# Kernel tuning notes

Measured on AMD Instinct MI355X. Metric: run time of the kernel, lower is better.

Reference implementation:

```python
import jax, jax.numpy as jnp
import numpy as np

AUX_LOSS_WEIGHT = 0.01
TOP_K = 2


def setup_inputs() -> dict:
    key = jax.random.key(0)
    k0, k1, k2, k3, k4 = jax.random.split(key, 5)
    B, S, H, I, E = 4, 2048, 1024, 2816, 8
    scale = 0.02
    x = jax.random.normal(k0, (B, S, H), dtype=jnp.float32)
    Wr = jax.random.normal(k1, (H, E), dtype=jnp.float32) * scale   # router
    Wg = jax.random.normal(k2, (E, H, I), dtype=jnp.float32) * scale  # gate proj per expert
    Wu = jax.random.normal(k3, (E, H, I), dtype=jnp.float32) * scale  # up proj per expert
    Wd = jax.random.normal(k4, (E, I, H), dtype=jnp.float32) * scale  # down proj per expert
    return {"x": x, "Wr": Wr, "Wg": Wg, "Wu": Wu, "Wd": Wd}


def reference(x, Wr, Wg, Wu, Wd):
    B, S, H = x.shape
    E = Wr.shape[1]
    xf = x.reshape(-1, H)                      # [T, H]

    # Router: softmax -> top-k -> renormalize top-k weights
    logits = xf @ Wr                           # [T, E]
    probs = jax.nn.softmax(logits, axis=-1)
    vals, idx = jax.lax.top_k(probs, TOP_K)    # [T, K]
    vals = vals / (vals.sum(axis=-1, keepdims=True) + 1e-9)

    # Aux load-balancing loss (matches torch: mean prob * mean one-hot load)
    oh = jax.nn.one_hot(idx, E, dtype=xf.dtype)        # [T, K, E]
    expert_load = oh.sum(axis=1).mean(axis=0)          # [E]
    expert_prob = probs.mean(axis=0)                   # [E]
    router_loss = E * jnp.sum(expert_prob * expert_load) * AUX_LOSS_WEIGHT

    # Per-token combine weight for each expert: c[t,e] = sum_k vals[t,k] * (idx[t,k]==e)
    comb = jnp.einsum('tk,tke->te', vals, oh)          # [T, E]

    # Loop over the small fixed set of experts (dense SwiGLU, masked-weighted combine;
    # identical math to gather -> expert -> weighted index_add scatter)
    def expert_step(acc, ew):
        wg, wu, wd, ce = ew                            # [H,I], [H,I], [I,H], [T]
        h = jax.nn.silu(xf @ wg) * (xf @ wu)           # [T, I]
        return acc + (h @ wd) * ce[:, None], None

    out, _ = jax.lax.scan(expert_step, jnp.zeros_like(xf), (Wg, Wu, Wd, comb.T))
    return out.reshape(B, S, H), router_loss
```

## Files before the change

### kernel.cpp

```cpp
#include <hip/hip_runtime.h>
#include <stdint.h>

#define T_TOK 8192
#define HD    1024
#define ID    2816
#define NE    8
#define RCAP  17408

typedef __bf16 bf16x8 __attribute__((ext_vector_type(8)));
typedef float  f32x4  __attribute__((ext_vector_type(4)));

__device__ __forceinline__ unsigned short f2bf(float f) {
  union { float f; unsigned u; } v; v.f = f;
  unsigned r = v.u + 0x7FFFu + ((v.u >> 16) & 1u);
  return (unsigned short)(r >> 16);
}

__device__ __forceinline__ void gl16(const void* g, void* l) {
  __builtin_amdgcn_global_load_lds((__attribute__((address_space(1))) void*)g,
                                   (__attribute__((address_space(3))) void*)l,
                                   16, 0, 0);
}

__global__ void k_transpose(const float* __restrict__ Wg, const float* __restrict__ Wu,
                            const float* __restrict__ Wd,
                            unsigned short* __restrict__ Wgt, unsigned short* __restrict__ Wut,
                            unsigned short* __restrict__ Wdt) {
  const int m = blockIdx.y;
  const float* src; unsigned short* dst; int R, C;
  if (m < 8)       { src = Wg + (size_t)m * HD * ID;        dst = Wgt + (size_t)m * HD * ID;        R = HD; C = ID; }
  else if (m < 16) { src = Wu + (size_t)(m - 8) * HD * ID;  dst = Wut + (size_t)(m - 8) * HD * ID;  R = HD; C = ID; }
  else             { src = Wd + (size_t)(m - 16) * HD * ID; dst = Wdt + (size_t)(m - 16) * HD * ID; R = ID; C = HD; }
  const int tc = C / 64;
  const int tr = blockIdx.x / tc, tcc = blockIdx.x % tc;
  const int r0 = tr * 64, c0 = tcc * 64;
  __shared__ __align__(16) unsigned short tl[64 * 64];
  const int t = threadIdx.x;
  const int rb = t >> 4;
  const int c4 = t & 15;
  const float* sp = src + (size_t)(r0 + rb * 4) * C + c0 + c4 * 4;
  float4 v[4];
#pragma unroll
  for (int i = 0; i < 4; ++i) v[i] = *(const float4*)(sp + (size_t)i * C);
  const float* vf = (const float*)v;
#pragma unroll
  for (int q = 0; q < 4; ++q) {
    const int c = c4 * 4 + q;
    ushort4 o;
    o.x = f2bf(vf[0 * 4 + q]); o.y = f2bf(vf[1 * 4 + q]);
    o.z = f2bf(vf[2 * 4 + q]); o.w = f2bf(vf[3 * 4 + q]);
    *(ushort4*)&tl[c * 64 + ((rb ^ (c & 15)) * 4)] = o;
  }
  __syncthreads();
  const int orow = t >> 2, seg = t & 3;
  __align__(16) unsigned short tmp[16];
#pragma unroll
  for (int mI = 0; mI < 4; ++mI) {
    const int s = seg * 4 + mI;
    *(ushort4*)&tmp[mI * 4] = *(const ushort4*)&tl[orow * 64 + ((s ^ (orow & 15)) * 4)];
  }
  unsigned short* dp = dst + (size_t)(c0 + orow) * R + r0 + seg * 16;
  ((uint4*)dp)[0] = ((const uint4*)tmp)[0];
  ((uint4*)dp)[1] = ((const uint4*)tmp)[1];
}

__global__ void k_router(const float* __restrict__ x, const float* __restrict__ Wr,
                         int* __restrict__ cnt, float* __restrict__ psum,
                         int* __restrict__ tok_e, float* __restrict__ tok_w,
                         unsigned short* __restrict__ xb) {
  __shared__ float bp[NE];
  __shared__ int bc[NE];
  const int tid = threadIdx.x;
  if (tid < NE) { bp[tid] = 0.f; bc[tid] = 0; }
  __syncthreads();
  const int lane = tid & 63, w = tid >> 6;
  const int t = blockIdx.x * 4 + w;
  float acc[NE] = {0.f, 0.f, 0.f, 0.f, 0.f, 0.f, 0.f, 0.f};
  for (int h = lane; h < HD; h += 64) {
    const float xv = x[(size_t)t * HD + h];
    xb[(size_t)t * HD + h] = f2bf(xv);
    const float4 w0 = *(const float4*)(Wr + h * 8);
    const float4 w1 = *(const float4*)(Wr + h * 8 + 4);
    acc[0] += xv * w0.x; acc[1] += xv * w0.y; acc[2] += xv * w0.z; acc[3] += xv * w0.w;
    acc[4] += xv * w1.x; acc[5] += xv * w1.y; acc[6] += xv * w1.z; acc[7] += xv * w1.w;
  }
#pragma unroll
  for (int e = 0; e < NE; ++e)
    for (int off = 32; off > 0; off >>= 1)
      acc[e] += __shfl_xor(acc[e], off, 64);
  if (lane == 0) {
    float mx = acc[0];
    for (int e = 1; e < NE; ++e) mx = fmaxf(mx, acc[e]);
    float p[NE], s = 0.f;
    for (int e = 0; e < NE; ++e) { p[e] = __expf(acc[e] - mx); s += p[e]; }
    const float inv = 1.f / s;
    for (int e = 0; e < NE; ++e) p[e] *= inv;
    int e0 = 0;
    for (int e = 1; e < NE; ++e) if (p[e] > p[e0]) e0 = e;
    int e1 = (e0 == 0) ? 1 : 0;
    for (int e = 0; e < NE; ++e) if (e != e0 && p[e] > p[e1]) e1 = e;
    const float v0 = p[e0], v1 = p[e1];
    const float invs = 1.f / (v0 + v1 + 1e-9f);
    tok_e[2 * t] = e0;          tok_e[2 * t + 1] = e1;
    tok_w[2 * t] = v0 * invs;   tok_w[2 * t + 1] = v1 * invs;
    atomicAdd(&bc[e0], 1); atomicAdd(&bc[e1], 1);
    for (int e = 0; e < NE; ++e) atomicAdd(&bp[e], p[e]);
  }
  __syncthreads();
  if (tid < NE) { atomicAdd(&cnt[tid], bc[tid]); atomicAdd(&psum[tid], bp[tid]); }
}

__global__ void k_offsets(const int* __restrict__ cnt, const float* __restrict__ psum,
                          int* __restrict__ offp, int* __restrict__ pair_tok,
                          float* __restrict__ pair_w, float* __restrict__ loss_out) {
  __shared__ int soff[NE + 1], scnt[NE];
  if (threadIdx.x == 0) {
    int o = 0;
    for (int e = 0; e < NE; ++e) {
      soff[e] = o; scnt[e] = cnt[e];
      o += (scnt[e] + 127) & ~127;
    }
    soff[NE] = o;
    for (int e = 0; e <= NE; ++e) offp[e] = soff[e];
    float loss = 0.f;
    for (int e = 0; e < NE; ++e) loss += psum[e] * (float)scnt[e];
    loss *= (float)NE * 0.01f / ((float)T_TOK * (float)T_TOK);
    *loss_out = loss;
  }
  __syncthreads();
  for (int e = 0; e < NE; ++e) {
    const int base = soff[e] + scnt[e];
    const int n = soff[e + 1] - base;
    for (int j = threadIdx.x; j < n; j += blockDim.x) {
      pair_tok[base + j] = -1;
      pair_w[base + j] = 0.f;
    }
  }
}

__global__ void k_scatter(const int* __restrict__ tok_e, const float* __restrict__ tok_w,
                          const int* __restrict__ offp, int* __restrict__ cursor,
                          int* __restrict__ pair_tok, float* __restrict__ pair_w,
                          int* __restrict__ inv_p) {
  const int t = blockIdx.x * 256 + threadIdx.x;
#pragma unroll
  for (int k = 0; k < 2; ++k) {
    const int e = tok_e[2 * t + k];
    const int pos = atomicAdd(&cursor[e], 1);
    const int idx = offp[e] + pos;
    pair_tok[idx] = t;
    pair_w[idx] = tok_w[2 * t + k];
    inv_p[2 * t + k] = idx;
  }
}

__launch_bounds__(256, 2)
__global__ void k_stage1(const unsigned short* __restrict__ xb,
                         const unsigned short* __restrict__ Wgt,
                         const unsigned short* __restrict__ Wut,
                         const int* __restrict__ offp,
                         const int* __restrict__ pair_tok,
                         unsigned short* __restrict__ act) {
  __shared__ __align__(16) unsigned short lA[8192];
  __shared__ __align__(16) unsigned short lBg[8192];
  __shared__ __align__(16) unsigned short lBu[8192];
  __shared__ int toks[128];

  const int row0 = blockIdx.y * 128;
  if (row0 >= offp[8]) return;
  int e = 0;
  while (offp[e + 1] <= row0) ++e;
  const int i0 = blockIdx.x * 128;
  const int tid = threadIdx.x;
  if (tid < 128) {
    const int tk = pair_tok[row0 + tid];
    toks[tid] = tk < 0 ? 0 : tk;
  }
  __syncthreads();

  const int lane = tid & 63, w = tid >> 6;
  const unsigned short* gA[4];
  const unsigned short* gBg[4];
  const unsigned short* gBu[4];
  unsigned ldso[4];
  const unsigned short* wgtE = Wgt + (size_t)e * ID * HD;
  const unsigned short* wutE = Wut + (size_t)e * ID * HD;
#pragma unroll
  for (int j = 0; j < 4; ++j) {
    const int row = (w * 4 + j) * 8 + (lane >> 3);
    const int kb = (lane & 7) ^ (row & 7);
    gA[j]  = xb + (size_t)toks[row] * HD + kb * 8;
    gBg[j] = wgtE + (size_t)(i0 + row) * HD + kb * 8;
    gBu[j] = wutE + (size_t)(i0 + row) * HD + kb * 8;
    ldso[j] = (unsigned)(w * 4 + j) * 512u;
  }

  const f32x4 zero = {0.f, 0.f, 0.f, 0.f};
  f32x4 accg[4][4], accu[4][4];
#pragma unroll
  for (int a = 0; a < 4; ++a)
#pragma unroll
    for (int b = 0; b < 4; ++b) { accg[a][b] = zero; accu[a][b] = zero; }

  const int wm = (w & 1) * 64, wn = (w >> 1) * 64;
  const int colm = lane & 15, quad = lane >> 4;

  for (int kt = 0; kt < HD / 64; ++kt) {
    __syncthreads();
    const int ko = kt * 64;
#pragma unroll
    for (int j = 0; j < 4; ++j) {
      gl16(gA[j] + ko,  &lA[ldso[j]]);
      gl16(gBg[j] + ko, &lBg[ldso[j]]);
      gl16(gBu[j] + ko, &lBu[ldso[j]]);
    }
    __syncthreads();
#pragma unroll
    for (int kk = 0; kk < 2; ++kk) {
      const int kbl = kk * 4 + quad;
      bf16x8 af[4], bg[4], bu[4];
#pragma unroll
      for (int mf = 0; mf < 4; ++mf) {
        const int r = wm + mf * 16 + colm;
        af[mf] = *(const bf16x8*)&lA[r * 64 + ((kbl ^ (r & 7)) * 8)];
      }
#pragma unroll
      for (int nf = 0; nf < 4; ++nf) {
        const int r = wn + nf * 16 + colm;
        const int o = r * 64 + ((kbl ^ (r & 7)) * 8);
        bg[nf] = *(const bf16x8*)&lBg[o];
        bu[nf] = *(const bf16x8*)&lBu[o];
      }
#pragma unroll
      for (int mf = 0; mf < 4; ++mf)
#pragma unroll
        for (int nf = 0; nf < 4; ++nf) {
          accg[mf][nf] = __builtin_amdgcn_mfma_f32_16x16x32_bf16(af[mf], bg[nf], accg[mf][nf], 0, 0, 0);
          accu[mf][nf] = __builtin_amdgcn_mfma_f32_16x16x32_bf16(af[mf], bu[nf], accu[mf][nf], 0, 0, 0);
        }
    }
  }

#pragma unroll
  for (int mf = 0; mf < 4; ++mf) {
#pragma unroll
    for (int r = 0; r < 4; ++r) {
      const int orow = row0 + wm + mf * 16 + quad * 4 + r;
      unsigned short* arow = act + (size_t)orow * ID + i0 + wn + colm;
#pragma unroll
      for (int nf = 0; nf < 4; ++nf) {
        const float g = accg[mf][nf][r];
        const float u = accu[mf][nf][r];
        const float h = (g / (1.f + __expf(-g))) * u;
        arow[nf * 16] = f2bf(h);
      }
    }
  }
}

template <bool USE_CONTRIB>
__launch_bounds__(256, 2)
__global__ void k_stage2_t(const unsigned short* __restrict__ act,
                           const unsigned short* __restrict__ Wdt,
                           const int* __restrict__ offp,
                           const int* __restrict__ pair_tok,
                           const float* __restrict__ pair_w,
                           float* __restrict__ contrib,
                           float* __restrict__ out) {
  __shared__ __align__(16) unsigned short lA[8192];
  __shared__ __align__(16) unsigned short lB[8192];
  __shared__ int toks[128];
  __shared__ float wts[128];

  const int row0 = blockIdx.y * 128;
  if (row0 >= offp[8]) return;
  int e = 0;
  while (offp[e + 1] <= row0) ++e;
  const int h0 = blockIdx.x * 128;
  const int tid = threadIdx.x;
  if (!USE_CONTRIB && tid < 128) {
    toks[tid] = pair_tok[row0 + tid];
    wts[tid] = pair_w[row0 + tid];
  }
  const int lane = tid & 63, w = tid >> 6;
  const unsigned short* gA[4];
  const unsigned short* gB[4];
  unsigned ldso[4];
  const unsigned short* wdE = Wdt + (size_t)e * HD * ID;
#pragma unroll
  for (int j = 0; j < 4; ++j) {
    const int row = (w * 4 + j) * 8 + (lane >> 3);
    const int kb = (lane & 7) ^ (row & 7);
    gA[j] = act + (size_t)(row0 + row) * ID + kb * 8;
    gB[j] = wdE + (size_t)(h0 + row) * ID + kb * 8;
    ldso[j] = (unsigned)(w * 4 + j) * 512u;
  }

  const f32x4 zero = {0.f, 0.f, 0.f, 0.f};
  f32x4 acc[4][4];
#pragma unroll
  for (int a = 0; a < 4; ++a)
#pragma unroll
    for (int b = 0; b < 4; ++b) acc[a][b] = zero;

  const int wm = (w & 1) * 64, wn = (w >> 1) * 64;
  const int colm = lane & 15, quad = lane >> 4;

  for (int kt = 0; kt < ID / 64; ++kt) {
    __syncthreads();
    const int ko = kt * 64;
#pragma unroll
    for (int j = 0; j < 4; ++j) {
      gl16(gA[j] + ko, &lA[ldso[j]]);
      gl16(gB[j] + ko, &lB[ldso[j]]);
    }
    __syncthreads();
#pragma unroll
    for (int kk = 0; kk < 2; ++kk) {
      const int kbl = kk * 4 + quad;
      bf16x8 af[4], bf_[4];
#pragma unroll
      for (int mf = 0; mf < 4; ++mf) {
        const int r = wm + mf * 16 + colm;
        af[mf] = *(const bf16x8*)&lA[r * 64 + ((kbl ^ (r & 7)) * 8)];
      }
#pragma unroll
      for (int nf = 0; nf < 4; ++nf) {
        const int r = wn + nf * 16 + colm;
        bf_[nf] = *(const bf16x8*)&lB[r * 64 + ((kbl ^ (r & 7)) * 8)];
      }
#pragma unroll
      for (int mf = 0; mf < 4; ++mf)
#pragma unroll
        for (int nf = 0; nf < 4; ++nf)
          acc[mf][nf] = __builtin_amdgcn_mfma_f32_16x16x32_bf16(af[mf], bf_[nf], acc[mf][nf], 0, 0, 0);
    }
  }

#pragma unroll
  for (int mf = 0; mf < 4; ++mf) {
#pragma unroll
    for (int r = 0; r < 4; ++r) {
      const int lrow = wm + mf * 16 + quad * 4 + r;
      if (USE_CONTRIB) {
        float* crow = contrib + (size_t)(row0 + lrow) * HD + h0 + wn + colm;
#pragma unroll
        for (int nf = 0; nf < 4; ++nf)
          crow[nf * 16] = acc[mf][nf][r];
      } else {
        const int t = toks[lrow];
        if (t < 0) continue;
        const float wt = wts[lrow];
        float* orow = out + (size_t)t * HD + h0 + wn + colm;
#pragma unroll
        for (int nf = 0; nf < 4; ++nf)
          atomicAdd(&orow[nf * 16], wt * acc[mf][nf][r]);
      }
    }
  }
}

__global__ void k_combine(const float* __restrict__ contrib, const int* __restrict__ inv_p,
                          const float* __restrict__ tok_w, float* __restrict__ out) {
  const int t = blockIdx.x;
  const int h4 = threadIdx.x;
  const int p0 = inv_p[2 * t], p1 = inv_p[2 * t + 1];
  const float w0 = tok_w[2 * t], w1 = tok_w[2 * t + 1];
  const float4 a = ((const float4*)(contrib + (size_t)p0 * HD))[h4];
  const float4 b = ((const float4*)(contrib + (size_t)p1 * HD))[h4];
  float4 o;
  o.x = w0 * a.x + w1 * b.x;
  o.y = w0 * a.y + w1 * b.y;
  o.z = w0 * a.z + w1 * b.z;
  o.w = w0 * a.w + w1 * b.w;
  ((float4*)(out + (size_t)t * HD))[h4] = o;
}

extern "C" void kernel_launch(void* const* d_in, const int* in_sizes, int n_in,
                              void* d_out, int out_size, void* d_ws, size_t ws_size,
                              hipStream_t stream) {
  const float* x  = (const float*)d_in[0];
  const float* Wr = (const float*)d_in[1];
  const float* Wg = (const float*)d_in[2];
  const float* Wu = (const float*)d_in[3];
  const float* Wd = (const float*)d_in[4];
  float* out = (float*)d_out;

  char* ws = (char*)d_ws;
  const size_t off_xb  = 256;
  const size_t sz_xb   = (size_t)T_TOK * HD * 2;
  const size_t sz_w    = (size_t)NE * HD * ID * 2;
  const size_t off_wgt = off_xb + sz_xb;
  const size_t off_wut = off_wgt + sz_w;
  const size_t off_wdt = off_wut + sz_w;
  const size_t off_act = off_wdt + sz_w;
  const size_t sz_act  = (size_t)RCAP * ID * 2;
  const size_t off_ptk = off_act + sz_act;
  const size_t off_pw  = off_ptk + (size_t)RCAP * 4;
  const size_t off_te  = off_pw + (size_t)RCAP * 4;
  const size_t off_tw  = off_te + (size_t)T_TOK * 2 * 4;
  const size_t off_ip  = off_tw + (size_t)T_TOK * 2 * 4;
  const size_t off_ctb = off_ip + (size_t)T_TOK * 2 * 4;
  const size_t need_base = off_ctb;
  const size_t need_full = off_ctb + (size_t)RCAP * HD * 4;
  if (ws_size < need_base) return;
  const bool use_contrib = (ws_size >= need_full);

  int*   cnt    = (int*)(ws + 0);
  float* psum   = (float*)(ws + 32);
  int*   cursor = (int*)(ws + 64);
  int*   offp   = (int*)(ws + 96);
  unsigned short* xb  = (unsigned short*)(ws + off_xb);
  unsigned short* Wgt = (unsigned short*)(ws + off_wgt);
  unsigned short* Wut = (unsigned short*)(ws + off_wut);
  unsigned short* Wdt = (unsigned short*)(ws + off_wdt);
  unsigned short* act = (unsigned short*)(ws + off_act);
  int*   pair_tok = (int*)(ws + off_ptk);
  float* pair_w   = (float*)(ws + off_pw);
  int*   tok_e    = (int*)(ws + off_te);
  float* tok_w    = (float*)(ws + off_tw);
  int*   inv_p    = (int*)(ws + off_ip);
  float* contrib  = (float*)(ws + off_ctb);

  hipMemsetAsync(ws, 0, 256, stream);
  if (!use_contrib)
    hipMemsetAsync(out, 0, (size_t)T_TOK * HD * sizeof(float), stream);

  k_transpose<<<dim3(704, 24), 256, 0, stream>>>(Wg, Wu, Wd, Wgt, Wut, Wdt);
  k_router<<<T_TOK / 4, 256, 0, stream>>>(x, Wr, cnt, psum, tok_e, tok_w, xb);
  k_offsets<<<1, 256, 0, stream>>>(cnt, psum, offp, pair_tok, pair_w, out + (size_t)T_TOK * HD);
  k_scatter<<<T_TOK / 256, 256, 0, stream>>>(tok_e, tok_w, offp, cursor, pair_tok, pair_w, inv_p);
  k_stage1<<<dim3(ID / 128, RCAP / 128), 256, 0, stream>>>(xb, Wgt, Wut, offp, pair_tok, act);
  if (use_contrib) {
    k_stage2_t<true><<<dim3(HD / 128, RCAP / 128), 256, 0, stream>>>(act, Wdt, offp, pair_tok, pair_w, contrib, out);
    k_combine<<<T_TOK, 256, 0, stream>>>(contrib, inv_p, tok_w, out);
  } else {
    k_stage2_t<false><<<dim3(HD / 128, RCAP / 128), 256, 0, stream>>>(act, Wdt, offp, pair_tok, pair_w, contrib, out);
  }
}
```

Measured before the change: 820.3 us.

## Fuse transpose and router, reorder GEMM grids, reuse weight buffer for contrib

```diff
diff --git a/kernel.cpp b/kernel.cpp
--- a/kernel.cpp
+++ b/kernel.cpp
@@ -6,6 +6,7 @@
 #define ID    2816
 #define NE    8
 #define RCAP  17408
+#define NYT   (RCAP / 128)
 
 typedef __bf16 bf16x8 __attribute__((ext_vector_type(8)));
 typedef float  f32x4  __attribute__((ext_vector_type(4)));
@@ -22,92 +23,94 @@
                                    16, 0, 0);
 }
 
-__global__ void k_transpose(const float* __restrict__ Wg, const float* __restrict__ Wu,
-                            const float* __restrict__ Wd,
-                            unsigned short* __restrict__ Wgt, unsigned short* __restrict__ Wut,
-                            unsigned short* __restrict__ Wdt) {
-  const int m = blockIdx.y;
-  const float* src; unsigned short* dst; int R, C;
-  if (m < 8)       { src = Wg + (size_t)m * HD * ID;        dst = Wgt + (size_t)m * HD * ID;        R = HD; C = ID; }
-  else if (m < 16) { src = Wu + (size_t)(m - 8) * HD * ID;  dst = Wut + (size_t)(m - 8) * HD * ID;  R = HD; C = ID; }
-  else             { src = Wd + (size_t)(m - 16) * HD * ID; dst = Wdt + (size_t)(m - 16) * HD * ID; R = ID; C = HD; }
-  const int tc = C / 64;
-  const int tr = blockIdx.x / tc, tcc = blockIdx.x % tc;
-  const int r0 = tr * 64, c0 = tcc * 64;
+__global__ void k_prep(const float* __restrict__ x, const float* __restrict__ Wr,
+                       const float* __restrict__ Wg, const float* __restrict__ Wu,
+                       const float* __restrict__ Wd,
+                       unsigned short* __restrict__ Wgt, unsigned short* __restrict__ Wut,
+                       unsigned short* __restrict__ Wdt, unsigned short* __restrict__ xb,
+                       int* __restrict__ cnt, float* __restrict__ psum,
+                       int* __restrict__ tok_e, float* __restrict__ tok_w) {
   __shared__ __align__(16) unsigned short tl[64 * 64];
-  const int t = threadIdx.x;
-  const int rb = t >> 4;
-  const int c4 = t & 15;
-  const float* sp = src + (size_t)(r0 + rb * 4) * C + c0 + c4 * 4;
-  float4 v[4];
-#pragma unroll
-  for (int i = 0; i < 4; ++i) v[i] = *(const float4*)(sp + (size_t)i * C);
-  const float* vf = (const float*)v;
-#pragma unroll
-  for (int q = 0; q < 4; ++q) {
-    const int c = c4 * 4 + q;
-    ushort4 o;
-    o.x = f2bf(vf[0 * 4 + q]); o.y = f2bf(vf[1 * 4 + q]);
-    o.z = f2bf(vf[2 * 4 + q]); o.w = f2bf(vf[3 * 4 + q]);
-    *(ushort4*)&tl[c * 64 + ((rb ^ (c & 15)) * 4)] = o;
-  }
-  __syncthreads();
-  const int orow = t >> 2, seg = t & 3;
-  __align__(16) unsigned short tmp[16];
-#pragma unroll
-  for (int mI = 0; mI < 4; ++mI) {
-    const int s = seg * 4 + mI;
-    *(ushort4*)&tmp[mI * 4] = *(const ushort4*)&tl[orow * 64 + ((s ^ (orow & 15)) * 4)];
-  }
-  unsigned short* dp = dst + (size_t)(c0 + orow) * R + r0 + seg * 16;
-  ((uint4*)dp)[0] = ((const uint4*)tmp)[0];
-  ((uint4*)dp)[1] = ((const uint4*)tmp)[1];
-}
-
-__global__ void k_router(const float* __restrict__ x, const float* __restrict__ Wr,
-                         int* __restrict__ cnt, float* __restrict__ psum,
-                         int* __restrict__ tok_e, float* __restrict__ tok_w,
-                         unsigned short* __restrict__ xb) {
   __shared__ float bp[NE];
   __shared__ int bc[NE];
-  const int tid = threadIdx.x;
-  if (tid < NE) { bp[tid] = 0.f; bc[tid] = 0; }
-  __syncthreads();
-  const int lane = tid & 63, w = tid >> 6;
-  const int t = blockIdx.x * 4 + w;
-  float acc[NE] = {0.f, 0.f, 0.f, 0.f, 0.f, 0.f, 0.f, 0.f};
-  for (int h = lane; h < HD; h += 64) {
-    const float xv = x[(size_t)t * HD + h];
-    xb[(size_t)t * HD + h] = f2bf(xv);
-    const float4 w0 = *(const float4*)(Wr + h * 8);
-    const float4 w1 = *(const float4*)(Wr + h * 8 + 4);
-    acc[0] += xv * w0.x; acc[1] += xv * w0.y; acc[2] += xv * w0.z; acc[3] += xv * w0.w;
-    acc[4] += xv * w1.x; acc[5] += xv * w1.y; acc[6] += xv * w1.z; acc[7] += xv * w1.w;
-  }
-#pragma unroll
-  for (int e = 0; e < NE; ++e)
-    for (int off = 32; off > 0; off >>= 1)
-      acc[e] += __shfl_xor(acc[e], off, 64);
-  if (lane == 0) {
-    float mx = acc[0];
-    for (int e = 1; e < NE; ++e) mx = fmaxf(mx, acc[e]);
-    float p[NE], s = 0.f;
-    for (int e = 0; e < NE; ++e) { p[e] = __expf(acc[e] - mx); s += p[e]; }
-    const float inv = 1.f / s;
-    for (int e = 0; e < NE; ++e) p[e] *= inv;
-    int e0 = 0;
-    for (int e = 1; e < NE; ++e) if (p[e] > p[e0]) e0 = e;
-    int e1 = (e0 == 0) ? 1 : 0;
-    for (int e = 0; e < NE; ++e) if (e != e0 && p[e] > p[e1]) e1 = e;
-    const float v0 = p[e0], v1 = p[e1];
-    const float invs = 1.f / (v0 + v1 + 1e-9f);
-    tok_e[2 * t] = e0;          tok_e[2 * t + 1] = e1;
-    tok_w[2 * t] = v0 * invs;   tok_w[2 * t + 1] = v1 * invs;
-    atomicAdd(&bc[e0], 1); atomicAdd(&bc[e1], 1);
-    for (int e = 0; e < NE; ++e) atomicAdd(&bp[e], p[e]);
-  }
-  __syncthreads();
-  if (tid < NE) { atomicAdd(&cnt[tid], bc[tid]); atomicAdd(&psum[tid], bp[tid]); }
+  const int bid = blockIdx.x;
+  const int t = threadIdx.x;
+
+  if (bid < 16896) {
+    const int m = bid / 704, bx = bid - m * 704;
+    const float* src; unsigned short* dst; int R, C;
+    if (m < 8)       { src = Wg + (size_t)m * HD * ID;        dst = Wgt + (size_t)m * HD * ID;        R = HD; C = ID; }
+    else if (m < 16) { src = Wu + (size_t)(m - 8) * HD * ID;  dst = Wut + (size_t)(m - 8) * HD * ID;  R = HD; C = ID; }
+    else             { src = Wd + (size_t)(m - 16) * HD * ID; dst = Wdt + (size_t)(m - 16) * HD * ID; R = ID; C = HD; }
+    const int tc = C / 64;
+    const int tr = bx / tc, tcc = bx % tc;
+    const int r0 = tr * 64, c0 = tcc * 64;
+    const int rb = t >> 4;
+    const int c4 = t & 15;
+    const float* sp = src + (size_t)(r0 + rb * 4) * C + c0 + c4 * 4;
+    float4 v[4];
+#pragma unroll
+    for (int i = 0; i < 4; ++i) v[i] = *(const float4*)(sp + (size_t)i * C);
+    const float* vf = (const float*)v;
+#pragma unroll
+    for (int q = 0; q < 4; ++q) {
+      const int c = c4 * 4 + q;
+      ushort4 o;
+      o.x = f2bf(vf[0 * 4 + q]); o.y = f2bf(vf[1 * 4 + q]);
+      o.z = f2bf(vf[2 * 4 + q]); o.w = f2bf(vf[3 * 4 + q]);
+      *(ushort4*)&tl[c * 64 + ((rb ^ (c & 15)) * 4)] = o;
+    }
+    __syncthreads();
+    const int orow = t >> 2, seg = t & 3;
+    __align__(16) unsigned short tmp[16];
+#pragma unroll
+    for (int mI = 0; mI < 4; ++mI) {
+      const int s = seg * 4 + mI;
+      *(ushort4*)&tmp[mI * 4] = *(const ushort4*)&tl[orow * 64 + ((s ^ (orow & 15)) * 4)];
+    }
+    unsigned short* dp = dst + (size_t)(c0 + orow) * R + r0 + seg * 16;
+    ((uint4*)dp)[0] = ((const uint4*)tmp)[0];
+    ((uint4*)dp)[1] = ((const uint4*)tmp)[1];
+  } else {
+    const int b = bid - 16896;
+    if (t < NE) { bp[t] = 0.f; bc[t] = 0; }
+    __syncthreads();
+    const int lane = t & 63, w = t >> 6;
+    const int tok = b * 4 + w;
+    float acc[NE] = {0.f, 0.f, 0.f, 0.f, 0.f, 0.f, 0.f, 0.f};
+    for (int h = lane; h < HD; h += 64) {
+      const float xv = x[(size_t)tok * HD + h];
+      xb[(size_t)tok * HD + h] = f2bf(xv);
+      const float4 w0 = *(const float4*)(Wr + h * 8);
+      const float4 w1 = *(const float4*)(Wr + h * 8 + 4);
+      acc[0] += xv * w0.x; acc[1] += xv * w0.y; acc[2] += xv * w0.z; acc[3] += xv * w0.w;
+      acc[4] += xv * w1.x; acc[5] += xv * w1.y; acc[6] += xv * w1.z; acc[7] += xv * w1.w;
+    }
+#pragma unroll
+    for (int e = 0; e < NE; ++e)
+      for (int off = 32; off > 0; off >>= 1)
+        acc[e] += __shfl_xor(acc[e], off, 64);
+    if (lane == 0) {
+      float mx = acc[0];
+      for (int e = 1; e < NE; ++e) mx = fmaxf(mx, acc[e]);
+      float p[NE], s = 0.f;
+      for (int e = 0; e < NE; ++e) { p[e] = __expf(acc[e] - mx); s += p[e]; }
+      const float inv = 1.f / s;
+      for (int e = 0; e < NE; ++e) p[e] *= inv;
+      int e0 = 0;
+      for (int e = 1; e < NE; ++e) if (p[e] > p[e0]) e0 = e;
+      int e1 = (e0 == 0) ? 1 : 0;
+      for (int e = 0; e < NE; ++e) if (e != e0 && p[e] > p[e1]) e1 = e;
+      const float v0 = p[e0], v1 = p[e1];
+      const float invs = 1.f / (v0 + v1 + 1e-9f);
+      tok_e[2 * tok] = e0;          tok_e[2 * tok + 1] = e1;
+      tok_w[2 * tok] = v0 * invs;   tok_w[2 * tok + 1] = v1 * invs;
+      atomicAdd(&bc[e0], 1); atomicAdd(&bc[e1], 1);
+      for (int e = 0; e < NE; ++e) atomicAdd(&bp[e], p[e]);
+    }
+    __syncthreads();
+    if (t < NE) { atomicAdd(&cnt[t], bc[t]); atomicAdd(&psum[t], bp[t]); }
+  }
 }
 
 __global__ void k_offsets(const int* __restrict__ cnt, const float* __restrict__ psum,
@@ -166,11 +169,13 @@
   __shared__ __align__(16) unsigned short lBu[8192];
   __shared__ int toks[128];
 
-  const int row0 = blockIdx.y * 128;
+  const int wg = blockIdx.x;
+  const int ytile = wg % NYT;
+  const int i0 = (wg / NYT) * 128;
+  const int row0 = ytile * 128;
   if (row0 >= offp[8]) return;
   int e = 0;
   while (offp[e + 1] <= row0) ++e;
-  const int i0 = blockIdx.x * 128;
   const int tid = threadIdx.x;
   if (tid < 128) {
     const int tk = pair_tok[row0 + tid];
@@ -258,30 +263,22 @@
   }
 }
 
-template <bool USE_CONTRIB>
 __launch_bounds__(256, 2)
-__global__ void k_stage2_t(const unsigned short* __restrict__ act,
-                           const unsigned short* __restrict__ Wdt,
-                           const int* __restrict__ offp,
-                           const int* __restrict__ pair_tok,
-                           const float* __restrict__ pair_w,
-                           float* __restrict__ contrib,
-                           float* __restrict__ out) {
+__global__ void k_stage2(const unsigned short* __restrict__ act,
+                         const unsigned short* __restrict__ Wdt,
+                         const int* __restrict__ offp,
+                         float* __restrict__ contrib) {
   __shared__ __align__(16) unsigned short lA[8192];
   __shared__ __align__(16) unsigned short lB[8192];
-  __shared__ int toks[128];
-  __shared__ float wts[128];
-
-  const int row0 = blockIdx.y * 128;
+
+  const int wg = blockIdx.x;
+  const int ytile = wg % NYT;
+  const int h0 = (wg / NYT) * 128;
+  const int row0 = ytile * 128;
   if (row0 >= offp[8]) return;
   int e = 0;
   while (offp[e + 1] <= row0) ++e;
-  const int h0 = blockIdx.x * 128;
   const int tid = threadIdx.x;
-  if (!USE_CONTRIB && tid < 128) {
-    toks[tid] = pair_tok[row0 + tid];
-    wts[tid] = pair_w[row0 + tid];
-  }
   const int lane = tid & 63, w = tid >> 6;
   const unsigned short* gA[4];
   const unsigned short* gB[4];
@@ -342,20 +339,10 @@
 #pragma unroll
     for (int r = 0; r < 4; ++r) {
       const int lrow = wm + mf * 16 + quad * 4 + r;
-      if (USE_CONTRIB) {
-        float* crow = contrib + (size_t)(row0 + lrow) * HD + h0 + wn + colm;
-#pragma unroll
-        for (int nf = 0; nf < 4; ++nf)
-          crow[nf * 16] = acc[mf][nf][r];
-      } else {
-        const int t = toks[lrow];
-        if (t < 0) continue;
-        const float wt = wts[lrow];
-        float* orow = out + (size_t)t * HD + h0 + wn + colm;
-#pragma unroll
-        for (int nf = 0; nf < 4; ++nf)
-          atomicAdd(&orow[nf * 16], wt * acc[mf][nf][r]);
-      }
+      float* crow = contrib + (size_t)(row0 + lrow) * HD + h0 + wn + colm;
+#pragma unroll
+      for (int nf = 0; nf < 4; ++nf)
+        crow[nf * 16] = acc[mf][nf][r];
     }
   }
 }
@@ -400,11 +387,8 @@
   const size_t off_te  = off_pw + (size_t)RCAP * 4;
   const size_t off_tw  = off_te + (size_t)T_TOK * 2 * 4;
   const size_t off_ip  = off_tw + (size_t)T_TOK * 2 * 4;
-  const size_t off_ctb = off_ip + (size_t)T_TOK * 2 * 4;
-  const size_t need_base = off_ctb;
-  const size_t need_full = off_ctb + (size_t)RCAP * HD * 4;
-  if (ws_size < need_base) return;
-  const bool use_contrib = (ws_size >= need_full);
+  const size_t need    = off_ip + (size_t)T_TOK * 2 * 4;
+  if (ws_size < need) return;
 
   int*   cnt    = (int*)(ws + 0);
   float* psum   = (float*)(ws + 32);
@@ -420,21 +404,15 @@
   int*   tok_e    = (int*)(ws + off_te);
   float* tok_w    = (float*)(ws + off_tw);
   int*   inv_p    = (int*)(ws + off_ip);
-  float* contrib  = (float*)(ws + off_ctb);
+  float* contrib  = (float*)(ws + off_wgt);
 
   hipMemsetAsync(ws, 0, 256, stream);
-  if (!use_contrib)
-    hipMemsetAsync(out, 0, (size_t)T_TOK * HD * sizeof(float), stream);
-
-  k_transpose<<<dim3(704, 24), 256, 0, stream>>>(Wg, Wu, Wd, Wgt, Wut, Wdt);
-  k_router<<<T_TOK / 4, 256, 0, stream>>>(x, Wr, cnt, psum, tok_e, tok_w, xb);
+
+  k_prep<<<16896 + T_TOK / 4, 256, 0, stream>>>(x, Wr, Wg, Wu, Wd, Wgt, Wut, Wdt, xb,
+                                                cnt, psum, tok_e, tok_w);
   k_offsets<<<1, 256, 0, stream>>>(cnt, psum, offp, pair_tok, pair_w, out + (size_t)T_TOK * HD);
   k_scatter<<<T_TOK / 256, 256, 0, stream>>>(tok_e, tok_w, offp, cursor, pair_tok, pair_w, inv_p);
-  k_stage1<<<dim3(ID / 128, RCAP / 128), 256, 0, stream>>>(xb, Wgt, Wut, offp, pair_tok, act);
-  if (use_contrib) {
-    k_stage2_t<true><<<dim3(HD / 128, RCAP / 128), 256, 0, stream>>>(act, Wdt, offp, pair_tok, pair_w, contrib, out);
-    k_combine<<<T_TOK, 256, 0, stream>>>(contrib, inv_p, tok_w, out);
-  } else {
-    k_stage2_t<false><<<dim3(HD / 128, RCAP / 128), 256, 0, stream>>>(act, Wdt, offp, pair_tok, pair_w, contrib, out);
-  }
-}
+  k_stage1<<<(ID / 128) * NYT, 256, 0, stream>>>(xb, Wgt, Wut, offp, pair_tok, act);
+  k_stage2<<<(HD / 128) * NYT, 256, 0, stream>>>(act, Wdt, offp, contrib);
+  k_combine<<<T_TOK, 256, 0, stream>>>(contrib, inv_p, tok_w, out);
+}
```

New measurement: 820.8 us. About the same (+0.1%).
